# Kernel tuning notes

Measured on AMD Instinct MI355X. Metric: run time of the kernel, lower is better.

The kernel has to match this reference:

```python
import jax, jax.numpy as jnp
import numpy as np

N = 4_000_000   # input points (nonzero voxels at tensor_stride 1)
B = 4           # batch size
G = 128         # voxel grid extent per axis at input stride
DIM = 3         # spatial dimension (init arg `dimension`)
STRIDE = 2      # kernel_size == stride == 2, dilation 1 -> coord // 2 pooling


def setup_inputs() -> dict:
    key = jax.random.key(0)
    k1, k2 = jax.random.split(key)
    batch_idx = jax.random.randint(k1, (N,), 0, B, dtype=jnp.int32)
    coords = jax.random.randint(k2, (N, DIM), 0, G, dtype=jnp.int32)
    # ME builds the "feature" tensor directly from the float coordinates
    coords_f = coords.astype(jnp.float32)
    return {"coords_f": coords_f, "batch_idx": batch_idx, "coords": coords,
            "grid_size": G}


def reference(coords_f, batch_idx, coords, grid_size):
    # Pooled (output) voxel per point: kernel==stride==2 => floor division.
    gs = grid_size // STRIDE                       # output grid extent per axis
    per_batch = gs ** DIM
    S = B * per_batch                              # dense output segment count

    out = coords // STRIDE                         # [N, 3] int
    lin = (out[:, 0] * gs + out[:, 1]) * gs + out[:, 2]
    seg = batch_idx * per_batch + lin              # [N] segment id in [0, S)

    ones = jnp.ones((coords_f.shape[0],), dtype=coords_f.dtype)
    # MinkowskiSumPooling on all-ones features = points per output voxel
    count = jax.ops.segment_sum(ones, seg, num_segments=S)          # [S]
    # MinkowskiGlobalSumPooling on ones = points per batch item
    glob = jax.ops.segment_sum(ones, batch_idx, num_segments=B)     # [B]

    seg_ids = jnp.arange(S)
    seg_batch = seg_ids // per_batch                                # [S]
    nonempty = count > 0
    # density = pool_xx / broadcast(pool_xx, glob_xx)
    density = jnp.where(nonempty, count / glob[seg_batch], 0.0)     # [S]

    # MinkowskiAvgPooling of coordinates -> per-voxel centroid
    csum = jax.ops.segment_sum(coords_f, seg, num_segments=S)       # [S, 3]
    safe_count = jnp.where(nonempty, count, 1.0)
    center = csum / safe_count[:, None]                             # [S, 3]

    # unpool(center) back to points, then sum-pool squared residuals
    mean_diff = coords_f - center[seg]                              # [N, 3]
    sqsum = jax.ops.segment_sum(mean_diff * mean_diff, seg, num_segments=S)
    variance = jnp.where(nonempty[:, None], sqsum / safe_count[:, None], 0.0)

    # Output-voxel coordinates (in original scale: multiples of STRIDE)
    rem = seg_ids % per_batch
    c0 = rem // (gs * gs)
    c1 = (rem // gs) % gs
    c2 = rem % gs
    out_coords = jnp.stack([c0, c1, c2], axis=-1).astype(coords_f.dtype) * STRIDE
    norm_center = jnp.where(nonempty[:, None], center - out_coords, 0.0)

    # ME.cat(density, variance, norm_center) -> [S, 2*DIM + 1]
    return jnp.concatenate([density[:, None], variance, norm_center], axis=1)
```

## Files before the change

kernel.cpp:

```cpp
#include <hip/hip_runtime.h>
#include <hip/hip_bf16.h>


#define BLOCK1 1024
#define PTS 8192
#define BUCKETS 256
#define SEG_SHIFT 12
#define SPB 4096
#define BLOCK2 1024
#define FBLOCK 256

__device__ __forceinline__ unsigned make_pay(int b, int x, int y, int z, int gs) {
    const int seg = (((b * gs + (x >> 1)) * gs + (y >> 1)) * gs) + (z >> 1);
    return ((unsigned)seg << 3) | ((unsigned)(x & 1) << 2)
         | ((unsigned)(y & 1) << 1) | (unsigned)(z & 1);
}

__global__ __launch_bounds__(BLOCK1, 8)
void partition_kernel(const int* __restrict__ bidx,
                      const int* __restrict__ coords,
                      const int* __restrict__ gptr,
                      unsigned* __restrict__ payload,
                      unsigned* __restrict__ g_cursor,
                      int N, int CAP) {
    __shared__ unsigned s_pay[PTS];
    __shared__ unsigned s_hist[BUCKETS];
    __shared__ unsigned s_base[BUCKETS];
    __shared__ unsigned s_old[BUCKETS];
    __shared__ unsigned s_cur[BUCKETS];

    const int tid = threadIdx.x;
    if (tid < BUCKETS) { s_hist[tid] = 0u; s_cur[tid] = 0u; }
    __syncthreads();

    const int gs = gptr[0] >> 1;
    const int base = blockIdx.x * PTS;
    const int cnt = min(PTS, N - base);

    const int4* __restrict__ bidx4 = (const int4*)bidx;
    const int4* __restrict__ crd4  = (const int4*)coords;

    #pragma unroll
    for (int g = 0; g < PTS / (BLOCK1 * 4); ++g) {
        const int p0 = base + (g * BLOCK1 + tid) * 4;
        if (p0 + 3 < N) {
            const int q = p0 >> 2;
            const int4 b4 = bidx4[q];
            const int4 c0 = crd4[3 * q + 0];
            const int4 c1 = crd4[3 * q + 1];
            const int4 c2 = crd4[3 * q + 2];
            atomicAdd(&s_hist[make_pay(b4.x, c0.x, c0.y, c0.z, gs) >> (SEG_SHIFT + 3)], 1u);
            atomicAdd(&s_hist[make_pay(b4.y, c0.w, c1.x, c1.y, gs) >> (SEG_SHIFT + 3)], 1u);
            atomicAdd(&s_hist[make_pay(b4.z, c1.z, c1.w, c2.x, gs) >> (SEG_SHIFT + 3)], 1u);
            atomicAdd(&s_hist[make_pay(b4.w, c2.y, c2.z, c2.w, gs) >> (SEG_SHIFT + 3)], 1u);
        } else {
            for (int p = p0; p < N && p < p0 + 4; ++p) {
                const unsigned pay = make_pay(bidx[p], coords[3 * p + 0],
                                              coords[3 * p + 1], coords[3 * p + 2], gs);
                atomicAdd(&s_hist[pay >> (SEG_SHIFT + 3)], 1u);
            }
        }
    }
    __syncthreads();

    {
        unsigned v = 0u;
        if (tid < BUCKETS) { v = s_hist[tid]; s_base[tid] = v; }
        __syncthreads();
        for (int off = 1; off < BUCKETS; off <<= 1) {
            unsigned t = 0u;
            if (tid < BUCKETS && tid >= off) t = s_base[tid - off];
            __syncthreads();
            if (tid < BUCKETS) s_base[tid] += t;
            __syncthreads();
        }
        if (tid < BUCKETS) {
            s_base[tid] -= v;
            s_old[tid] = atomicAdd(&g_cursor[tid], v);
        }
        __syncthreads();
    }

    #pragma unroll
    for (int g = 0; g < PTS / (BLOCK1 * 4); ++g) {
        const int p0 = base + (g * BLOCK1 + tid) * 4;
        if (p0 + 3 < N) {
            const int q = p0 >> 2;
            const int4 b4 = bidx4[q];
            const int4 c0 = crd4[3 * q + 0];
            const int4 c1 = crd4[3 * q + 1];
            const int4 c2 = crd4[3 * q + 2];
            unsigned pay, bk, r;
            pay = make_pay(b4.x, c0.x, c0.y, c0.z, gs); bk = pay >> (SEG_SHIFT + 3);
            r = atomicAdd(&s_cur[bk], 1u); s_pay[s_base[bk] + r] = pay;
            pay = make_pay(b4.y, c0.w, c1.x, c1.y, gs); bk = pay >> (SEG_SHIFT + 3);
            r = atomicAdd(&s_cur[bk], 1u); s_pay[s_base[bk] + r] = pay;
            pay = make_pay(b4.z, c1.z, c1.w, c2.x, gs); bk = pay >> (SEG_SHIFT + 3);
            r = atomicAdd(&s_cur[bk], 1u); s_pay[s_base[bk] + r] = pay;
            pay = make_pay(b4.w, c2.y, c2.z, c2.w, gs); bk = pay >> (SEG_SHIFT + 3);
            r = atomicAdd(&s_cur[bk], 1u); s_pay[s_base[bk] + r] = pay;
        } else {
            for (int p = p0; p < N && p < p0 + 4; ++p) {
                const unsigned pay = make_pay(bidx[p], coords[3 * p + 0],
                                              coords[3 * p + 1], coords[3 * p + 2], gs);
                const unsigned bk = pay >> (SEG_SHIFT + 3);
                const unsigned r = atomicAdd(&s_cur[bk], 1u);
                s_pay[s_base[bk] + r] = pay;
            }
        }
    }
    __syncthreads();

    for (int j = tid; j < cnt; j += BLOCK1) {
        const unsigned p = s_pay[j];
        const unsigned bk = p >> (SEG_SHIFT + 3);
        const unsigned off = s_old[bk] + ((unsigned)j - s_base[bk]);
        if (off < (unsigned)CAP)
            payload[(size_t)bk * CAP + off] = p;
    }
}

__global__ __launch_bounds__(BLOCK2)
void stats_kernel(const unsigned* __restrict__ payload,
                  const unsigned* __restrict__ g_cursor,
                  float* __restrict__ out, int CAP) {
    __shared__ unsigned fine[SPB];
    __shared__ float s_stage[BLOCK2 * 7];
    __shared__ unsigned s_g[64];

    const int tid = threadIdx.x;
    const int k = blockIdx.x;

    for (int s = tid; s < SPB; s += BLOCK2) fine[s] = 0u;
    if (tid < 64) s_g[tid] = g_cursor[(k & ~63) + tid];
    __syncthreads();
    for (int o = 32; o > 0; o >>= 1) {
        if (tid < o) s_g[tid] += s_g[tid + o];
        __syncthreads();
    }
    const float ginv = 1.0f / (float)s_g[0];

    unsigned cnt = g_cursor[k];
    if (cnt > (unsigned)CAP) cnt = (unsigned)CAP;
    const uint4* __restrict__ pay4 = (const uint4*)(payload + (size_t)k * CAP);
    const unsigned n4 = cnt >> 2;

    for (unsigned j = tid; j < n4; j += BLOCK2) {
        const uint4 p = pay4[j];
        atomicAdd(&fine[(p.x >> 3) & (SPB - 1)],
                  (1u << 24) | ((p.x & 4u) << 14) | ((p.x & 2u) << 7) | (p.x & 1u));
        atomicAdd(&fine[(p.y >> 3) & (SPB - 1)],
                  (1u << 24) | ((p.y & 4u) << 14) | ((p.y & 2u) << 7) | (p.y & 1u));
        atomicAdd(&fine[(p.z >> 3) & (SPB - 1)],
                  (1u << 24) | ((p.z & 4u) << 14) | ((p.z & 2u) << 7) | (p.z & 1u));
        atomicAdd(&fine[(p.w >> 3) & (SPB - 1)],
                  (1u << 24) | ((p.w & 4u) << 14) | ((p.w & 2u) << 7) | (p.w & 1u));
    }
    for (unsigned j = (n4 << 2) + tid; j < cnt; j += BLOCK2) {
        const unsigned p = payload[(size_t)k * CAP + j];
        atomicAdd(&fine[(p >> 3) & (SPB - 1)],
                  (1u << 24) | ((p & 4u) << 14) | ((p & 2u) << 7) | (p & 1u));
    }
    __syncthreads();

    for (int t = 0; t < SPB; t += BLOCK2) {
        const unsigned a = fine[t + tid];
        const int c = (int)(a >> 24);
        float d0 = 0.f, vx = 0.f, vy = 0.f, vz = 0.f, mx = 0.f, my = 0.f, mz = 0.f;
        if (c > 0) {
            const float inv = 1.0f / (float)c;
            mx = (float)((a >> 16) & 0xffu) * inv;
            my = (float)((a >> 8) & 0xffu) * inv;
            mz = (float)(a & 0xffu) * inv;
            vx = mx - mx * mx;
            vy = my - my * my;
            vz = mz - mz * mz;
            d0 = (float)c * ginv;
        }
        float* st = &s_stage[tid * 7];
        st[0] = d0;
        st[1] = vx; st[2] = vy; st[3] = vz;
        st[4] = mx; st[5] = my; st[6] = mz;
        __syncthreads();

        const float4* src = (const float4*)s_stage;
        float4* dst = (float4*)(out + ((size_t)k * SPB + t) * 7);
        #pragma unroll
        for (int j = 0; j < (BLOCK2 * 7) / (4 * BLOCK2) + 1; ++j) {
            const int idx = j * BLOCK2 + tid;
            if (idx < (BLOCK2 * 7) / 4) dst[idx] = src[idx];
        }
        __syncthreads();
    }
}

__global__ __launch_bounds__(FBLOCK)
void accum_kernel(const int* __restrict__ bidx,
                  const int* __restrict__ coords,
                  const int* __restrict__ gptr,
                  unsigned* __restrict__ acc, int astride,
                  int* __restrict__ glob, int N) {
    __shared__ int gcnt[4];
    if (threadIdx.x < 4) gcnt[threadIdx.x] = 0;
    __syncthreads();
    const int gs = gptr[0] >> 1;
    int l0 = 0, l1 = 0, l2 = 0, l3 = 0;
    const int stride = gridDim.x * blockDim.x;
    for (int i = blockIdx.x * blockDim.x + threadIdx.x; i < N; i += stride) {
        const int b  = bidx[i];
        const int cx = coords[3 * i + 0];
        const int cy = coords[3 * i + 1];
        const int cz = coords[3 * i + 2];
        const int seg = (((b * gs + (cx >> 1)) * gs + (cy >> 1)) * gs) + (cz >> 1);
        const unsigned val = (1u << 24)
                           | ((unsigned)(cx & 1) << 16)
                           | ((unsigned)(cy & 1) << 8)
                           |  (unsigned)(cz & 1);
        atomicAdd(&acc[(size_t)seg * astride], val);
        l0 += (b == 0); l1 += (b == 1); l2 += (b == 2); l3 += (b == 3);
    }
    if (l0) atomicAdd(&gcnt[0], l0);
    if (l1) atomicAdd(&gcnt[1], l1);
    if (l2) atomicAdd(&gcnt[2], l2);
    if (l3) atomicAdd(&gcnt[3], l3);
    __syncthreads();
    if (threadIdx.x < 4 && gcnt[threadIdx.x] != 0)
        atomicAdd(&glob[threadIdx.x], gcnt[threadIdx.x]);
}

__global__ __launch_bounds__(FBLOCK)
void finalize_kernel(const unsigned* __restrict__ acc, int astride,
                     const int* __restrict__ glob,
                     float* __restrict__ out, int S, int pbShift) {
    const int s = blockIdx.x * blockDim.x + threadIdx.x;
    if (s >= S) return;
    const unsigned a = acc[(size_t)s * astride];
    const int b = s >> pbShift;
    const int c = (int)(a >> 24);
    float d0 = 0.f, vx = 0.f, vy = 0.f, vz = 0.f, mx = 0.f, my = 0.f, mz = 0.f;
    if (c > 0) {
        const float inv = 1.0f / (float)c;
        mx = (float)((a >> 16) & 0xffu) * inv;
        my = (float)((a >> 8) & 0xffu) * inv;
        mz = (float)(a & 0xffu) * inv;
        vx = mx - mx * mx; vy = my - my * my; vz = mz - mz * mz;
        d0 = (float)c / (float)glob[b];
    }
    float* row = out + (size_t)s * 7;
    row[0] = d0;
    row[1] = vx; row[2] = vy; row[3] = vz;
    row[4] = mx; row[5] = my; row[6] = mz;
}

extern "C" void kernel_launch(void* const* d_in, const int* in_sizes, int n_in,
                              void* d_out, int out_size, void* d_ws, size_t ws_size,
                              hipStream_t stream) {
    const int* bidx   = (const int*)d_in[1];
    const int* coords = (const int*)d_in[2];
    const int* gptr   = (const int*)d_in[3];

    const int N = in_sizes[1];
    const int S = out_size / 7;
    const int per_batch = S / 4;

    const int NpB = (N + BUCKETS - 1) / BUCKETS;
    const int CAP = ((NpB + NpB / 8 + 64) + 63) & ~63;
    const size_t need = 1024 + (size_t)BUCKETS * (size_t)CAP * 4u;

    const bool fast = (S == (BUCKETS * SPB)) && (per_batch == (S / 4)) &&
                      (per_batch / SPB == 64) && (ws_size >= need) && (N > 0);

    if (fast) {
        unsigned* g_cursor = (unsigned*)d_ws;
        unsigned* payload  = (unsigned*)((char*)d_ws + 1024);
        hipMemsetAsync(d_ws, 0, 1024, stream);

        const int blocks = (N + PTS - 1) / PTS;
        partition_kernel<<<blocks, BLOCK1, 0, stream>>>(
            bidx, coords, gptr, payload, g_cursor, N, CAP);
        stats_kernel<<<BUCKETS, BLOCK2, 0, stream>>>(
            payload, g_cursor, (float*)d_out, CAP);
    } else {
        int pbShift = 0;
        while ((1 << pbShift) < per_batch) ++pbShift;
        int* glob = (int*)d_ws;
        const size_t accBytes = (size_t)S * sizeof(unsigned);
        unsigned* acc;
        int astride;
        if (ws_size >= accBytes + 64) {
            acc = (unsigned*)((char*)d_ws + 64);
            astride = 1;
            hipMemsetAsync(d_ws, 0, 64 + accBytes, stream);
        } else {
            acc = (unsigned*)d_out;
            astride = 7;
            hipMemsetAsync(d_out, 0, (size_t)out_size * sizeof(float), stream);
            hipMemsetAsync(d_ws, 0, 64, stream);
        }
        int accBlocks = (N + FBLOCK - 1) / FBLOCK;
        if (accBlocks > 2048) accBlocks = 2048;
        accum_kernel<<<accBlocks, FBLOCK, 0, stream>>>(bidx, coords, gptr,
                                                       acc, astride, glob, N);
        const int finBlocks = (S + FBLOCK - 1) / FBLOCK;
        finalize_kernel<<<finBlocks, FBLOCK, 0, stream>>>(acc, astride, glob,
                                                          (float*)d_out, S, pbShift);
    }
}
```

Before: 148.6 us.

## Keep partition payloads in registers and scatter directly to global buckets

The partition kernel now computes each thread's 8 payloads once and keeps them in registers. Before, it re-read the inputs for a second pass and staged payloads in a shared-memory array sorted by an in-block prefix scan. The scan and the staging buffer are gone. Each point gets its slot from a shared atomic cursor and is written straight to its global bucket. This removes the duplicate global loads, several barriers and 32KB of LDS, but the global writes are no longer grouped by bucket, so coalescing may be worse, and the launch bounds drop from 8 to 2 blocks per CU.

New measurement: 156.1 us. +5.0%, slower.

```diff
diff --git a/kernel.cpp b/kernel.cpp
--- a/kernel.cpp
+++ b/kernel.cpp
@@ -3,7 +3,8 @@
 
 
 #define BLOCK1 1024
-#define PTS 8192
+#define PPT 8
+#define PTS (BLOCK1 * PPT)
 #define BUCKETS 256
 #define SEG_SHIFT 12
 #define SPB 4096
@@ -16,16 +17,14 @@
          | ((unsigned)(y & 1) << 1) | (unsigned)(z & 1);
 }
 
-__global__ __launch_bounds__(BLOCK1, 8)
+__global__ __launch_bounds__(BLOCK1, 2)
 void partition_kernel(const int* __restrict__ bidx,
                       const int* __restrict__ coords,
                       const int* __restrict__ gptr,
                       unsigned* __restrict__ payload,
                       unsigned* __restrict__ g_cursor,
                       int N, int CAP) {
-    __shared__ unsigned s_pay[PTS];
     __shared__ unsigned s_hist[BUCKETS];
-    __shared__ unsigned s_base[BUCKETS];
     __shared__ unsigned s_old[BUCKETS];
     __shared__ unsigned s_cur[BUCKETS];
 
@@ -35,13 +34,13 @@
 
     const int gs = gptr[0] >> 1;
     const int base = blockIdx.x * PTS;
-    const int cnt = min(PTS, N - base);
 
     const int4* __restrict__ bidx4 = (const int4*)bidx;
     const int4* __restrict__ crd4  = (const int4*)coords;
 
+    unsigned pay[PPT];
     #pragma unroll
-    for (int g = 0; g < PTS / (BLOCK1 * 4); ++g) {
+    for (int g = 0; g < PPT / 4; ++g) {
         const int p0 = base + (g * BLOCK1 + tid) * 4;
         if (p0 + 3 < N) {
             const int q = p0 >> 2;
@@ -49,74 +48,41 @@
             const int4 c0 = crd4[3 * q + 0];
             const int4 c1 = crd4[3 * q + 1];
             const int4 c2 = crd4[3 * q + 2];
-            atomicAdd(&s_hist[make_pay(b4.x, c0.x, c0.y, c0.z, gs) >> (SEG_SHIFT + 3)], 1u);
-            atomicAdd(&s_hist[make_pay(b4.y, c0.w, c1.x, c1.y, gs) >> (SEG_SHIFT + 3)], 1u);
-            atomicAdd(&s_hist[make_pay(b4.z, c1.z, c1.w, c2.x, gs) >> (SEG_SHIFT + 3)], 1u);
-            atomicAdd(&s_hist[make_pay(b4.w, c2.y, c2.z, c2.w, gs) >> (SEG_SHIFT + 3)], 1u);
+            pay[g * 4 + 0] = make_pay(b4.x, c0.x, c0.y, c0.z, gs);
+            pay[g * 4 + 1] = make_pay(b4.y, c0.w, c1.x, c1.y, gs);
+            pay[g * 4 + 2] = make_pay(b4.z, c1.z, c1.w, c2.x, gs);
+            pay[g * 4 + 3] = make_pay(b4.w, c2.y, c2.z, c2.w, gs);
         } else {
-            for (int p = p0; p < N && p < p0 + 4; ++p) {
-                const unsigned pay = make_pay(bidx[p], coords[3 * p + 0],
-                                              coords[3 * p + 1], coords[3 * p + 2], gs);
-                atomicAdd(&s_hist[pay >> (SEG_SHIFT + 3)], 1u);
+            #pragma unroll
+            for (int j = 0; j < 4; ++j) {
+                const int p = p0 + j;
+                pay[g * 4 + j] = (p < N)
+                    ? make_pay(bidx[p], coords[3 * p + 0],
+                               coords[3 * p + 1], coords[3 * p + 2], gs)
+                    : 0xFFFFFFFFu;
             }
         }
     }
-    __syncthreads();
-
-    {
-        unsigned v = 0u;
-        if (tid < BUCKETS) { v = s_hist[tid]; s_base[tid] = v; }
-        __syncthreads();
-        for (int off = 1; off < BUCKETS; off <<= 1) {
-            unsigned t = 0u;
-            if (tid < BUCKETS && tid >= off) t = s_base[tid - off];
-            __syncthreads();
-            if (tid < BUCKETS) s_base[tid] += t;
-            __syncthreads();
-        }
-        if (tid < BUCKETS) {
-            s_base[tid] -= v;
-            s_old[tid] = atomicAdd(&g_cursor[tid], v);
-        }
-        __syncthreads();
-    }
-
     #pragma unroll
-    for (int g = 0; g < PTS / (BLOCK1 * 4); ++g) {
-        const int p0 = base + (g * BLOCK1 + tid) * 4;
-        if (p0 + 3 < N) {
-            const int q = p0 >> 2;
-            const int4 b4 = bidx4[q];
-            const int4 c0 = crd4[3 * q + 0];
-            const int4 c1 = crd4[3 * q + 1];
-            const int4 c2 = crd4[3 * q + 2];
-            unsigned pay, bk, r;
-            pay = make_pay(b4.x, c0.x, c0.y, c0.z, gs); bk = pay >> (SEG_SHIFT + 3);
-            r = atomicAdd(&s_cur[bk], 1u); s_pay[s_base[bk] + r] = pay;
-            pay = make_pay(b4.y, c0.w, c1.x, c1.y, gs); bk = pay >> (SEG_SHIFT + 3);
-            r = atomicAdd(&s_cur[bk], 1u); s_pay[s_base[bk] + r] = pay;
-            pay = make_pay(b4.z, c1.z, c1.w, c2.x, gs); bk = pay >> (SEG_SHIFT + 3);
-            r = atomicAdd(&s_cur[bk], 1u); s_pay[s_base[bk] + r] = pay;
-            pay = make_pay(b4.w, c2.y, c2.z, c2.w, gs); bk = pay >> (SEG_SHIFT + 3);
-            r = atomicAdd(&s_cur[bk], 1u); s_pay[s_base[bk] + r] = pay;
-        } else {
-            for (int p = p0; p < N && p < p0 + 4; ++p) {
-                const unsigned pay = make_pay(bidx[p], coords[3 * p + 0],
-                                              coords[3 * p + 1], coords[3 * p + 2], gs);
-                const unsigned bk = pay >> (SEG_SHIFT + 3);
-                const unsigned r = atomicAdd(&s_cur[bk], 1u);
-                s_pay[s_base[bk] + r] = pay;
-            }
-        }
-    }
-    __syncthreads();
-
-    for (int j = tid; j < cnt; j += BLOCK1) {
-        const unsigned p = s_pay[j];
-        const unsigned bk = p >> (SEG_SHIFT + 3);
-        const unsigned off = s_old[bk] + ((unsigned)j - s_base[bk]);
-        if (off < (unsigned)CAP)
-            payload[(size_t)bk * CAP + off] = p;
+    for (int j = 0; j < PPT; ++j)
+        if (pay[j] != 0xFFFFFFFFu)
+            atomicAdd(&s_hist[pay[j] >> (SEG_SHIFT + 3)], 1u);
+    __syncthreads();
+
+    if (tid < BUCKETS)
+        s_old[tid] = atomicAdd(&g_cursor[tid], s_hist[tid]);
+    __syncthreads();
+
+    #pragma unroll
+    for (int j = 0; j < PPT; ++j) {
+        const unsigned p = pay[j];
+        if (p != 0xFFFFFFFFu) {
+            const unsigned bk = p >> (SEG_SHIFT + 3);
+            const unsigned r = atomicAdd(&s_cur[bk], 1u);
+            const unsigned off = s_old[bk] + r;
+            if (off < (unsigned)CAP)
+                payload[(size_t)bk * CAP + off] = p;
+        }
     }
 }
 
```
